# Optimization experiments

Hardware: AMD Instinct MI355X
Metric: run time of the kernel (lower is better)

## Reference

```python
import jax, jax.numpy as jnp
import numpy as np

L = 50
N_INIT = 3.5      # initial radius n
N_STEP = 0.5      # n_step
NUM_ADJ_PARM = 0.1
NUM_CANDS = 256   # candidate radii n + k*n_step


def _leaky(x):
    return jax.nn.leaky_relu(x, negative_slope=0.01)


def _conv(x, w, b):
    y = jax.lax.conv_general_dilated(x, w, (1, 1), 'VALID',
                                     dimension_numbers=('NCHW', 'OIHW', 'NCHW'))
    return y + b[None, :, None, None]


def _maxpool2(x):
    return jax.lax.reduce_window(x, -jnp.inf, jax.lax.max,
                                 (1, 1, 2, 2), (1, 1, 2, 2), 'VALID')


def _sage(x, adj, w_rel, b_rel, w_root):
    # PyG DenseSAGEConv: lin_rel(mean-agg) + lin_root(x), normalize=False
    agg = adj @ x
    deg = jnp.clip(jnp.sum(adj, axis=-1, keepdims=True), 1.0, None)
    return (agg / deg) @ w_rel.T + b_rel + x @ w_root.T


def _build_adj(h):
    # fused pairwise euclidean distance + radius threshold with retry:
    # smallest radius in {n + k*n_step} whose (directed) edge count >= 0.1*N
    g = h @ h.T                                   # [N,N] gram
    sq = jnp.diag(g)
    dist = jnp.sqrt(jnp.maximum(sq[:, None] - 2.0 * g + sq[None, :], 0.0))
    n = h.shape[0]
    eye = jnp.eye(n, dtype=bool)
    d_sorted = jnp.sort(jnp.where(eye, jnp.inf, dist).reshape(-1))
    cands = N_INIT + N_STEP * jnp.arange(NUM_CANDS, dtype=dist.dtype)
    counts = jnp.searchsorted(d_sorted, cands)    # edges with dist < cand
    thr = cands[jnp.argmax(counts >= NUM_ADJ_PARM * n)]
    A = ((dist < thr) & (~eye)).astype(h.dtype)
    return jax.lax.stop_gradient(A)               # edge list is non-diff in torch too


def _diff_pool(z, a, s):
    # PyG dense_diff_pool (link + entropy losses; only link loss l1 is returned)
    s = jax.nn.softmax(s, axis=-1)
    x = s.T @ z
    adj = s.T @ a @ s
    l1 = jnp.linalg.norm(a - s @ s.T) / (a.shape[0] * a.shape[1])
    return x, adj, l1


def setup_inputs() -> dict:
    key = jax.random.key(0)
    ks = jax.random.split(key, 19)
    def w(k, shape, scale=0.05):
        return scale * jax.random.normal(k, shape, dtype=jnp.float32)
    N = 4096  # bag size / number of graph nodes
    return {
        'x': jax.random.normal(ks[0], (1, N, 1, 28, 28), dtype=jnp.float32),
        'conv1_w': w(ks[1], (20, 1, 5, 5)),
        'conv1_b': w(ks[2], (20,)),
        'conv2_w': w(ks[3], (50, 20, 5, 5)),
        'conv2_b': w(ks[4], (50,)),
        'fc_w': w(ks[5], (50, 800)),
        'fc_b': w(ks[6], (50,)),
        'embd_rel_w': w(ks[7], (50, 50)),
        'embd_rel_b': w(ks[8], (50,)),
        'embd_root_w': w(ks[9], (50, 50)),
        'pool_rel_w': w(ks[10], (1, 50)),
        'pool_rel_b': w(ks[11], (1,)),
        'pool_root_w': w(ks[12], (1, 50)),
        'mlp_w': w(ks[13], (1, 1)),
        'mlp_b': w(ks[14], (1,)),
        'lin1_w': w(ks[15], (25, 50)),
        'lin1_b': w(ks[16], (25,)),
        'lin2_w': w(ks[17], (2, 25)),
        'lin2_b': w(ks[18], (2,)),
    }


def reference(x, conv1_w, conv1_b, conv2_w, conv2_b, fc_w, fc_b,
              embd_rel_w, embd_rel_b, embd_root_w,
              pool_rel_w, pool_rel_b, pool_root_w,
              mlp_w, mlp_b, lin1_w, lin1_b, lin2_w, lin2_b):
    xi = x[0]                                             # squeeze(0): [N,1,28,28]
    h = _maxpool2(jax.nn.relu(_conv(xi, conv1_w, conv1_b)))   # [N,20,12,12]
    h = _maxpool2(jax.nn.relu(_conv(h, conv2_w, conv2_b)))    # [N,50,4,4]
    h = h.reshape(h.shape[0], -1)                         # [N,800]
    h = jax.nn.relu(h @ fc_w.T + fc_b)                    # [N,50]
    A = _build_adj(h)                                     # [N,N] dense adjacency
    Z = _leaky(_sage(h, A, embd_rel_w, embd_rel_b, embd_root_w))   # [N,50]
    S = _leaky(_sage(h, A, pool_rel_w, pool_rel_b, pool_root_w))   # [N,1]
    S = _leaky(S @ mlp_w.T + mlp_b)                       # [N,1]
    Xp, adjp, l1 = _diff_pool(Z, A, S)                    # [1,50], [1,1]
    Xp = _leaky(_sage(Xp, adjp, embd_rel_w, embd_rel_b, embd_root_w))  # reuses gnn_embd
    v = Xp.reshape(-1)                                    # [50]
    v = _leaky(v @ lin1_w.T + lin1_b)                     # [25]
    v = _leaky(v @ lin2_w.T + lin2_b)                     # [2]
    p = jax.nn.softmax(v, axis=0)
    return jnp.max(p), jnp.argmax(p), l1
```

## Files before the change

### kernel.cpp

```cpp
#include <hip/hip_runtime.h>
#include <hip/hip_bf16.h>

#define AGG_OFF     0u
#define DEG_OFF     819200u
#define XP_OFF      835584u
#define HIST_OFF    835840u
#define SCAL_OFF    836992u
#define S_OFF       837120u
#define H_OFF       1048576u
#define HT_OFF      1867776u
#define SQ_OFF      2686976u

__global__ __launch_bounds__(256) void mil_init(unsigned int* __restrict__ w)
{
    w[(size_t)blockIdx.x * 256u + threadIdx.x] = 0u;
}

__global__ __launch_bounds__(256) void mil_cnn(
    const float* __restrict__ x, const float* __restrict__ w1, const float* __restrict__ b1,
    const float* __restrict__ w2, const float* __restrict__ b2,
    const float* __restrict__ fcw, const float* __restrict__ fcb,
    float* __restrict__ hout, float* __restrict__ hT, float* __restrict__ sqout)
{
    __shared__ __align__(16) float img[784];
    __shared__ float w1s[500];
    __shared__ float b1s[20];
    __shared__ float b2s[50];
    __shared__ __align__(16) float pool1[20*144];
    __shared__ float w2s[50*4*25];
    __shared__ __align__(16) float pool2[800];
    __shared__ float hloc[50];

    const int n = blockIdx.x;
    const int t = threadIdx.x;

    const float* xin = x + (size_t)n * 784;
    for (int i = t; i < 784; i += 256) img[i] = xin[i];
    for (int i = t; i < 500; i += 256) w1s[i] = w1[i];
    if (t < 20) b1s[t] = b1[t];
    { int u = t - 32; if (u >= 0 && u < 50) b2s[u] = b2[u]; }
    __syncthreads();

    if (t < 240) {
        const int c = t / 12, py = t % 12;
        float wr[25];
#pragma unroll
        for (int k = 0; k < 25; k++) wr[k] = w1s[c*25 + k];
        float acc0[24], acc1[24];
#pragma unroll
        for (int i = 0; i < 24; i++) { acc0[i] = 0.f; acc1[i] = 0.f; }
#pragma unroll
        for (int ky = 0; ky < 5; ky++) {
            const int yr = 2*py + ky;
            float ra[28], rb[28];
#pragma unroll
            for (int i = 0; i < 28; i++) ra[i] = img[yr*28 + i];
#pragma unroll
            for (int i = 0; i < 28; i++) rb[i] = img[yr*28 + 28 + i];
#pragma unroll
            for (int kx = 0; kx < 5; kx++) {
                const float wv = wr[ky*5 + kx];
#pragma unroll
                for (int xo = 0; xo < 24; xo++) {
                    acc0[xo] = fmaf(ra[xo+kx], wv, acc0[xo]);
                    acc1[xo] = fmaf(rb[xo+kx], wv, acc1[xo]);
                }
            }
        }
        const float bias = b1s[c];
#pragma unroll
        for (int px = 0; px < 12; px++) {
            float v = fmaxf(fmaxf(acc0[2*px], acc0[2*px+1]),
                            fmaxf(acc1[2*px], acc1[2*px+1]));
            pool1[c*144 + py*12 + px] = fmaxf(v + bias, 0.f);
        }
    }
    __syncthreads();

    float acc2[16];
#pragma unroll
    for (int i = 0; i < 16; i++) acc2[i] = 0.f;
    const int c2 = t / 4, py2 = t % 4;
    for (int cig = 0; cig < 5; cig++) {
        __syncthreads();
        for (int idx = t; idx < 5000; idx += 256) {
            const int cc = idx / 100, rem = idx % 100;
            w2s[idx] = w2[cc*500 + cig*100 + rem];
        }
        __syncthreads();
        if (t < 200) {
#pragma unroll
            for (int cl = 0; cl < 4; cl++) {
                const int cig4 = cig*4 + cl;
#pragma unroll
                for (int ky = 0; ky < 5; ky++) {
                    const int r = 2*py2 + ky;
                    float ra[12], rb[12];
#pragma unroll
                    for (int i = 0; i < 12; i++) ra[i] = pool1[cig4*144 + r*12 + i];
#pragma unroll
                    for (int i = 0; i < 12; i++) rb[i] = pool1[cig4*144 + (r+1)*12 + i];
#pragma unroll
                    for (int kx = 0; kx < 5; kx++) {
                        const float wv = w2s[(c2*4 + cl)*25 + ky*5 + kx];
#pragma unroll
                        for (int xo = 0; xo < 8; xo++) {
                            acc2[xo]   = fmaf(ra[xo+kx], wv, acc2[xo]);
                            acc2[8+xo] = fmaf(rb[xo+kx], wv, acc2[8+xo]);
                        }
                    }
                }
            }
        }
    }
    __syncthreads();
    if (t < 200) {
        const float bias = b2s[c2];
#pragma unroll
        for (int px = 0; px < 4; px++) {
            float v = fmaxf(fmaxf(acc2[2*px], acc2[2*px+1]),
                            fmaxf(acc2[8+2*px], acc2[8+2*px+1]));
            pool2[c2*16 + py2*4 + px] = fmaxf(v + bias, 0.f);
        }
    }
    __syncthreads();

    {
        const int wv = t >> 6, lane = t & 63;
        for (int o = wv; o < 50; o += 4) {
            float acc = 0.f;
#pragma unroll
            for (int r = 0; r < 13; r++) {
                const int k = r*64 + lane;
                if (k < 800) acc = fmaf(fcw[o*800 + k], pool2[k], acc);
            }
#pragma unroll
            for (int off = 32; off > 0; off >>= 1) acc += __shfl_xor(acc, off);
            if (lane == 0) hloc[o] = fmaxf(acc + fcb[o], 0.f);
        }
    }
    __syncthreads();
    if (t < 50) {
        const float v = hloc[t];
        hout[(size_t)n*50 + t] = v;
        hT[(size_t)t*4096 + n] = v;
    }
    if (t < 64) {
        float s = (t < 50) ? hloc[t]*hloc[t] : 0.f;
#pragma unroll
        for (int off = 32; off > 0; off >>= 1) s += __shfl_xor(s, off);
        if (t == 0) sqout[n] = s;
    }
}

__global__ __launch_bounds__(256) void mil_colsum(
    const float* __restrict__ hT, float* __restrict__ S)
{
    __shared__ float red[4];
    const int d = blockIdx.x, t = threadIdx.x;
    float s = 0.f;
    for (int nn = t; nn < 4096; nn += 256) s += hT[(size_t)d*4096 + nn];
#pragma unroll
    for (int off = 32; off > 0; off >>= 1) s += __shfl_xor(s, off);
    if ((t & 63) == 0) red[t >> 6] = s;
    __syncthreads();
    if (t == 0) S[d] = red[0] + red[1] + red[2] + red[3];
}

__global__ __launch_bounds__(256, 3) void mil_hist(
    const float* __restrict__ hT, const float* __restrict__ sq,
    unsigned int* __restrict__ hist)
{
    __shared__ __align__(16) float hiT[6400];
    __shared__ __align__(16) float hjT[6400];
    __shared__ float sqi[128], sqj[128];
    __shared__ unsigned int lh[257];

    const int t = threadIdx.x;
    const int i0 = blockIdx.x * 128, j0 = blockIdx.y * 128;

    for (int idx = t; idx < 6400; idx += 256) {
        const int c = idx >> 7, l = idx & 127;
        hiT[idx] = hT[(size_t)c*4096 + i0 + l];
        hjT[idx] = hT[(size_t)c*4096 + j0 + l];
    }
    if (t < 128) { sqi[t] = sq[i0 + t]; sqj[t] = sq[j0 + t]; }
    for (int idx = t; idx < 257; idx += 256) lh[idx] = 0;
    __syncthreads();

    const int ti = t >> 4, tj = t & 15;
    float acc[8][8];
#pragma unroll
    for (int a = 0; a < 8; a++)
#pragma unroll
        for (int b = 0; b < 8; b++) acc[a][b] = 0.f;

    for (int c = 0; c < 50; c++) {
        const float4 a0 = *(const float4*)&hiT[c*128 + ti*8];
        const float4 a1 = *(const float4*)&hiT[c*128 + ti*8 + 4];
        const float4 b0 = *(const float4*)&hjT[c*128 + tj*8];
        const float4 b1 = *(const float4*)&hjT[c*128 + tj*8 + 4];
        const float aa[8] = {a0.x,a0.y,a0.z,a0.w,a1.x,a1.y,a1.z,a1.w};
        const float bb[8] = {b0.x,b0.y,b0.z,b0.w,b1.x,b1.y,b1.z,b1.w};
#pragma unroll
        for (int a = 0; a < 8; a++)
#pragma unroll
            for (int b = 0; b < 8; b++)
                acc[a][b] = fmaf(aa[a], bb[b], acc[a][b]);
    }

    unsigned int cnt0 = 0;
#pragma unroll
    for (int a = 0; a < 8; a++) {
#pragma unroll
        for (int b = 0; b < 8; b++) {
            const int gi = i0 + ti*8 + a, gj = j0 + tj*8 + b;
            if (gi == gj) continue;
            const float d2 = sqi[ti*8+a] + sqj[tj*8+b] - 2.f*acc[a][b];
            const float d = sqrtf(fmaxf(d2, 0.f));
            int k = (int)floorf((d - 3.5f)*2.f) + 1;
            k = k < 0 ? 0 : (k > 256 ? 256 : k);
            if (k > 0   && d <  3.5f + 0.5f*(float)(k-1)) k--;
            if (k < 256 && d >= 3.5f + 0.5f*(float)k)     k++;
            if (k == 0) cnt0++;
            else atomicAdd(&lh[k], 1u);
        }
    }
#pragma unroll
    for (int off = 32; off > 0; off >>= 1) cnt0 += __shfl_xor(cnt0, off);
    if ((t & 63) == 0 && cnt0) atomicAdd(&lh[0], cnt0);
    __syncthreads();
    for (int idx = t; idx < 257; idx += 256)
        if (lh[idx]) atomicAdd(&hist[idx], lh[idx]);
}

__global__ void mil_scan(const unsigned int* __restrict__ hist, int* __restrict__ scal)
{
    if (threadIdx.x == 0) {
        unsigned long long cum = 0, nz = 0;
        int kc = -1;
        for (int k = 0; k < 256; k++) {
            cum += hist[k];
            if (kc < 0 && cum >= 410ull) { kc = k; nz = cum; }
        }
        if (kc < 0) { kc = 0; nz = hist[0]; }
        scal[0] = kc;
        scal[1] = (int)nz;
        scal[2] = (nz * 2ull > 16773120ull) ? 1 : 0;
    }
}

__global__ __launch_bounds__(256, 3) void mil_agg(
    const float* __restrict__ h, const float* __restrict__ hT, const float* __restrict__ sq,
    const int* __restrict__ scal, float* __restrict__ agg, float* __restrict__ deg)
{
    __shared__ __align__(16) float hiT[3200];
    __shared__ __align__(16) float hjT[3200];
    __shared__ float sqi[64], sqj[64];
    __shared__ __align__(16) float hsub[4096];
    __shared__ __align__(16) unsigned char mk[4096];

    const int t = threadIdx.x;
    const int i0 = blockIdx.x * 64;
    const float thr = 3.5f + 0.5f * (float)scal[0];
    const bool inv = (scal[2] != 0);

    for (int idx = t; idx < 3200; idx += 256) {
        const int c = idx >> 6, l = idx & 63;
        hiT[idx] = hT[(size_t)c*4096 + i0 + l];
    }
    if (t < 64) sqi[t] = sq[i0 + t];

    const int ti = t >> 4, tj = t & 15;
    const int il = t >> 2, dq = t & 3;
    float accum[16];
#pragma unroll
    for (int i = 0; i < 16; i++) accum[i] = 0.f;
    int degc = 0;

    for (int js = 0; js < 8; js++) {
        const int j0 = blockIdx.y * 512 + js * 64;
        __syncthreads();
        for (int idx = t; idx < 3200; idx += 256) {
            const int c = idx >> 6, l = idx & 63;
            hjT[idx] = hT[(size_t)c*4096 + j0 + l];
        }
        for (int idx = t; idx < 4096; idx += 256) {
            const int jj = idx >> 6, d = idx & 63;
            hsub[idx] = (d < 50) ? h[(size_t)(j0 + jj)*50 + d] : 0.f;
        }
        if (t < 64) sqj[t] = sq[j0 + t];
        __syncthreads();

        float acc[4][4];
#pragma unroll
        for (int a = 0; a < 4; a++)
#pragma unroll
            for (int b = 0; b < 4; b++) acc[a][b] = 0.f;
        for (int c = 0; c < 50; c++) {
            const float4 av = *(const float4*)&hiT[c*64 + ti*4];
            const float4 bv = *(const float4*)&hjT[c*64 + tj*4];
            const float aa[4] = {av.x, av.y, av.z, av.w};
            const float bb[4] = {bv.x, bv.y, bv.z, bv.w};
#pragma unroll
            for (int a = 0; a < 4; a++)
#pragma unroll
                for (int b = 0; b < 4; b++)
                    acc[a][b] = fmaf(aa[a], bb[b], acc[a][b]);
        }

#pragma unroll
        for (int b = 0; b < 4; b++) {
            unsigned char ob[4];
#pragma unroll
            for (int a = 0; a < 4; a++) {
                const int gi = i0 + ti*4 + a, gj = j0 + tj*4 + b;
                const float d2 = sqi[ti*4+a] + sqj[tj*4+b] - 2.f*acc[a][b];
                const float dd = sqrtf(fmaxf(d2, 0.f));
                const bool edge = (dd < thr);
                ob[a] = (gi != gj && (edge != inv)) ? 1 : 0;
            }
            *(uchar4*)&mk[(tj*4+b)*64 + ti*4] = make_uchar4(ob[0], ob[1], ob[2], ob[3]);
        }
        __syncthreads();

        for (int jj = 0; jj < 64; jj++) {
            const bool e = (mk[jj*64 + il] != 0);
            if (!__any(e)) continue;
            const float m = e ? 1.f : 0.f;
            if (e && dq == 0) degc++;
#pragma unroll
            for (int q = 0; q < 4; q++) {
                const float4 hv = *(const float4*)&hsub[jj*64 + dq*16 + q*4];
                accum[q*4+0] = fmaf(m, hv.x, accum[q*4+0]);
                accum[q*4+1] = fmaf(m, hv.y, accum[q*4+1]);
                accum[q*4+2] = fmaf(m, hv.z, accum[q*4+2]);
                accum[q*4+3] = fmaf(m, hv.w, accum[q*4+3]);
            }
        }
    }

    const int node = i0 + il;
#pragma unroll
    for (int q = 0; q < 4; q++)
#pragma unroll
        for (int rr = 0; rr < 4; rr++) {
            const int d = dq*16 + q*4 + rr;
            if (d < 50 && accum[q*4+rr] != 0.f)
                atomicAdd(&agg[(size_t)node*50 + d], accum[q*4+rr]);
        }
    if (dq == 0 && degc) atomicAdd(&deg[node], (float)degc);
}

__global__ __launch_bounds__(256) void mil_sage(
    const float* __restrict__ h, const float* __restrict__ agg, const float* __restrict__ deg,
    const float* __restrict__ S, const int* __restrict__ scal,
    const float* __restrict__ relw, const float* __restrict__ relb,
    const float* __restrict__ rootw, float* __restrict__ Xp)
{
    __shared__ float relT[2500];
    __shared__ float rootT[2500];
    __shared__ float rb[50];
    __shared__ float hn[250], mn[250], zb[250];
    const int t = threadIdx.x;
    const int nb = blockIdx.x * 5;
    const bool inv = (scal[2] != 0);

    for (int idx = t; idx < 2500; idx += 256) {
        const int d = idx / 50, c = idx % 50;
        relT[c*50 + d]  = relw[idx];
        rootT[c*50 + d] = rootw[idx];
    }
    if (t < 50) rb[t] = relb[t];
    if (t < 250) {
        const int nl = t / 50, d = t % 50;
        const int node = nb + nl;
        if (node < 4096) {
            const float hv = h[(size_t)node*50 + d];
            float av = agg[(size_t)node*50 + d];
            float dg = deg[node];
            if (inv) { av = S[d] - hv - av; dg = 4095.f - dg; }
            hn[t] = hv;
            mn[t] = av / fmaxf(dg, 1.f);
        } else { hn[t] = 0.f; mn[t] = 0.f; }
    }
    __syncthreads();
    if (t < 250) {
        const int nl = t / 50, d = t % 50;
        float z = rb[d];
        for (int c = 0; c < 50; c++) {
            z = fmaf(mn[nl*50 + c], relT[c*50 + d], z);
            z = fmaf(hn[nl*50 + c], rootT[c*50 + d], z);
        }
        z = z > 0.f ? z : 0.01f * z;
        zb[t] = (nb + nl < 4096) ? z : 0.f;
    }
    __syncthreads();
    if (t < 50) {
        float s = 0.f;
#pragma unroll
        for (int nl = 0; nl < 5; nl++) s += zb[nl*50 + t];
        atomicAdd(&Xp[t], s);
    }
}

__global__ void mil_final(
    const float* __restrict__ Xp, const int* __restrict__ scal,
    const float* __restrict__ relw, const float* __restrict__ relb,
    const float* __restrict__ rootw,
    const float* __restrict__ l1w, const float* __restrict__ l1b,
    const float* __restrict__ l2w, const float* __restrict__ l2b,
    float* __restrict__ out)
{
    __shared__ float xp[50], x2[50], v1[25], v2[2];
    const int t = threadIdx.x;
    if (t < 50) xp[t] = Xp[t];
    __syncthreads();
    const float adjp = (float)scal[1];
    const float dmax = fmaxf(adjp, 1.f);
    if (t < 50) {
        float z = relb[t];
        for (int c = 0; c < 50; c++) {
            const float mnc = (adjp * xp[c]) / dmax;
            z = fmaf(mnc,   relw[t*50 + c], z);
            z = fmaf(xp[c], rootw[t*50 + c], z);
        }
        x2[t] = z > 0.f ? z : 0.01f*z;
    }
    __syncthreads();
    if (t < 25) {
        float v = l1b[t];
        for (int c = 0; c < 50; c++) v = fmaf(l1w[t*50 + c], x2[c], v);
        v1[t] = v > 0.f ? v : 0.01f*v;
    }
    __syncthreads();
    if (t < 2) {
        float v = l2b[t];
        for (int c = 0; c < 25; c++) v = fmaf(l2w[t*25 + c], v1[c], v);
        v2[t] = v > 0.f ? v : 0.01f*v;
    }
    __syncthreads();
    if (t == 0) {
        const float a = v2[0], b = v2[1];
        const float mx = fmaxf(a, b);
        const float e0 = expf(a - mx), e1 = expf(b - mx);
        const float s = e0 + e1;
        const float p0 = e0 / s, p1 = e1 / s;
        const float pm = fmaxf(p0, p1);
        const float am = (p1 > p0) ? 1.f : 0.f;
        const int nnz = scal[1];
        const float l1v = sqrtf((float)(16777216 - nnz)) / 16777216.f;
        out[0] = pm;
        out[1] = am;
        out[2] = l1v;
    }
}

extern "C" void kernel_launch(void* const* d_in, const int* in_sizes, int n_in,
                              void* d_out, int out_size, void* d_ws, size_t ws_size,
                              hipStream_t stream)
{
    (void)in_sizes; (void)n_in; (void)out_size; (void)ws_size;
    const float* x     = (const float*)d_in[0];
    const float* w1    = (const float*)d_in[1];
    const float* b1    = (const float*)d_in[2];
    const float* w2    = (const float*)d_in[3];
    const float* b2    = (const float*)d_in[4];
    const float* fcw   = (const float*)d_in[5];
    const float* fcb   = (const float*)d_in[6];
    const float* relw  = (const float*)d_in[7];
    const float* relb  = (const float*)d_in[8];
    const float* rootw = (const float*)d_in[9];
    const float* l1w   = (const float*)d_in[15];
    const float* l1b   = (const float*)d_in[16];
    const float* l2w   = (const float*)d_in[17];
    const float* l2b   = (const float*)d_in[18];

    char* ws = (char*)d_ws;
    float* agg = (float*)(ws + AGG_OFF);
    float* deg = (float*)(ws + DEG_OFF);
    float* Xp  = (float*)(ws + XP_OFF);
    unsigned int* hist = (unsigned int*)(ws + HIST_OFF);
    int* scal  = (int*)(ws + SCAL_OFF);
    float* S   = (float*)(ws + S_OFF);
    float* h   = (float*)(ws + H_OFF);
    float* hT  = (float*)(ws + HT_OFF);
    float* sq  = (float*)(ws + SQ_OFF);

    mil_init<<<818, 256, 0, stream>>>((unsigned int*)d_ws);
    mil_cnn<<<4096, 256, 0, stream>>>(x, w1, b1, w2, b2, fcw, fcb, h, hT, sq);
    mil_colsum<<<50, 256, 0, stream>>>(hT, S);
    mil_hist<<<dim3(32, 32), 256, 0, stream>>>(hT, sq, hist);
    mil_scan<<<1, 64, 0, stream>>>(hist, scal);
    mil_agg<<<dim3(64, 8), 256, 0, stream>>>(h, hT, sq, scal, agg, deg);
    mil_sage<<<820, 256, 0, stream>>>(h, agg, deg, S, scal, relw, relb, rootw, Xp);
    mil_final<<<1, 64, 0, stream>>>(Xp, scal, relw, relb, rootw,
                                    l1w, l1b, l2w, l2b, (float*)d_out);
}
```

Baseline: 548.4 us.

## Run conv2 on MFMA with split-bf16 and aggregate histogram atomics per wavefront

Rewrites the second convolution as an implicit GEMM on bf16 MFMA instructions. Each fp32 operand is split into a high and a low bf16 part, and three MFMAs per tile approximate fp32 accuracy. A new prep kernel converts the conv2 weights into padded hi/lo bf16 arrays, which replaces the per-block shared-memory staging of weights. The histogram kernel now merges lanes that hit the same bin with ballot and popcount before each shared atomic, to cut atomic contention. The split-bf16 scheme drops the lo*lo term, so small numeric differences could shift radius-bin edges.

Measured after the change: 624.9 us. 14.0% more time.

```diff
diff --git a/kernel.cpp b/kernel.cpp
--- a/kernel.cpp
+++ b/kernel.cpp
@@ -10,15 +10,44 @@
 #define H_OFF       1048576u
 #define HT_OFF      1867776u
 #define SQ_OFF      2686976u
+#define W2H_OFF     2703360u
+#define W2L_OFF     2785280u
+
+typedef __attribute__((ext_vector_type(8))) short short8;
+typedef __attribute__((ext_vector_type(4))) float f32x4;
+
+__device__ __forceinline__ unsigned short f32_to_bf16_rne(float v) {
+    unsigned u = __float_as_uint(v);
+    unsigned r = u + 0x7FFFu + ((u >> 16) & 1u);
+    return (unsigned short)(r >> 16);
+}
+__device__ __forceinline__ float bf16_to_f32(unsigned short s) {
+    return __uint_as_float(((unsigned)s) << 16);
+}
 
 __global__ __launch_bounds__(256) void mil_init(unsigned int* __restrict__ w)
 {
     w[(size_t)blockIdx.x * 256u + threadIdx.x] = 0u;
 }
 
-__global__ __launch_bounds__(256) void mil_cnn(
+__global__ __launch_bounds__(256) void mil_wprep(
+    const float* __restrict__ w2, unsigned short* __restrict__ w2h,
+    unsigned short* __restrict__ w2l)
+{
+    const int gid = blockIdx.x * 256 + threadIdx.x;
+    const int k = gid % 640;
+    const int c = gid / 640;
+    const float v = (c < 50 && k < 500) ? w2[c*500 + k] : 0.f;
+    const unsigned short h = f32_to_bf16_rne(v);
+    const unsigned short l = f32_to_bf16_rne(v - bf16_to_f32(h));
+    w2h[gid] = h;
+    w2l[gid] = l;
+}
+
+__global__ __launch_bounds__(256, 3) void mil_cnn(
     const float* __restrict__ x, const float* __restrict__ w1, const float* __restrict__ b1,
-    const float* __restrict__ w2, const float* __restrict__ b2,
+    const unsigned short* __restrict__ w2h, const unsigned short* __restrict__ w2l,
+    const float* __restrict__ b2,
     const float* __restrict__ fcw, const float* __restrict__ fcb,
     float* __restrict__ hout, float* __restrict__ hT, float* __restrict__ sqout)
 {
@@ -27,9 +56,9 @@
     __shared__ float b1s[20];
     __shared__ float b2s[50];
     __shared__ __align__(16) float pool1[20*144];
-    __shared__ float w2s[50*4*25];
     __shared__ __align__(16) float pool2[800];
     __shared__ float hloc[50];
+    __shared__ int tabk[640];
 
     const int n = blockIdx.x;
     const int t = threadIdx.x;
@@ -39,6 +68,14 @@
     for (int i = t; i < 500; i += 256) w1s[i] = w1[i];
     if (t < 20) b1s[t] = b1[t];
     { int u = t - 32; if (u >= 0 && u < 50) b2s[u] = b2[u]; }
+    for (int kidx = t; kidx < 640; kidx += 256) {
+        int off = -1;
+        if (kidx < 500) {
+            const int ci = kidx / 25, r = kidx % 25;
+            off = ci*144 + (r/5)*12 + (r%5);
+        }
+        tabk[kidx] = off;
+    }
     __syncthreads();
 
     if (t < 240) {
@@ -77,50 +114,51 @@
     }
     __syncthreads();
 
-    float acc2[16];
-#pragma unroll
-    for (int i = 0; i < 16; i++) acc2[i] = 0.f;
-    const int c2 = t / 4, py2 = t % 4;
-    for (int cig = 0; cig < 5; cig++) {
-        __syncthreads();
-        for (int idx = t; idx < 5000; idx += 256) {
-            const int cc = idx / 100, rem = idx % 100;
-            w2s[idx] = w2[cc*500 + cig*100 + rem];
-        }
-        __syncthreads();
-        if (t < 200) {
-#pragma unroll
-            for (int cl = 0; cl < 4; cl++) {
-                const int cig4 = cig*4 + cl;
-#pragma unroll
-                for (int ky = 0; ky < 5; ky++) {
-                    const int r = 2*py2 + ky;
-                    float ra[12], rb[12];
-#pragma unroll
-                    for (int i = 0; i < 12; i++) ra[i] = pool1[cig4*144 + r*12 + i];
-#pragma unroll
-                    for (int i = 0; i < 12; i++) rb[i] = pool1[cig4*144 + (r+1)*12 + i];
-#pragma unroll
-                    for (int kx = 0; kx < 5; kx++) {
-                        const float wv = w2s[(c2*4 + cl)*25 + ky*5 + kx];
-#pragma unroll
-                        for (int xo = 0; xo < 8; xo++) {
-                            acc2[xo]   = fmaf(ra[xo+kx], wv, acc2[xo]);
-                            acc2[8+xo] = fmaf(rb[xo+kx], wv, acc2[8+xo]);
-                        }
-                    }
+    {
+        const int lane = t & 63, wv = t >> 6;
+        const int cL = lane & 15, g = lane >> 4;
+        const int srow = wv*16 + cL;
+        const int soff = (srow >> 3)*12 + (srow & 7);
+        f32x4 acc[4];
+#pragma unroll
+        for (int nn = 0; nn < 4; ++nn) acc[nn] = (f32x4){0.f, 0.f, 0.f, 0.f};
+
+        for (int kk = 0; kk < 20; ++kk) {
+            const int k0 = kk*32 + g*8;
+            short8 ah, al;
+#pragma unroll
+            for (int e = 0; e < 8; ++e) {
+                const int off = tabk[k0 + e];
+                const float v = (off >= 0) ? pool1[off + soff] : 0.f;
+                const unsigned short hh = f32_to_bf16_rne(v);
+                const unsigned short ll = f32_to_bf16_rne(v - bf16_to_f32(hh));
+                ah[e] = (short)hh;
+                al[e] = (short)ll;
+            }
+#pragma unroll
+            for (int nn = 0; nn < 4; ++nn) {
+                const int bo = (nn*16 + cL)*640 + k0;
+                const short8 bh = *(const short8*)(w2h + bo);
+                const short8 bl = *(const short8*)(w2l + bo);
+                acc[nn] = __builtin_amdgcn_mfma_f32_16x16x32_bf16(al, bh, acc[nn], 0, 0, 0);
+                acc[nn] = __builtin_amdgcn_mfma_f32_16x16x32_bf16(ah, bl, acc[nn], 0, 0, 0);
+                acc[nn] = __builtin_amdgcn_mfma_f32_16x16x32_bf16(ah, bh, acc[nn], 0, 0, 0);
+            }
+        }
+#pragma unroll
+        for (int nn = 0; nn < 4; ++nn) {
+            const float x0 = fmaxf(acc[nn].x, acc[nn].y);
+            const float x1 = fmaxf(acc[nn].z, acc[nn].w);
+            const float y0 = fmaxf(x0, __shfl_xor(x0, 32));
+            const float y1 = fmaxf(x1, __shfl_xor(x1, 32));
+            if (lane < 32) {
+                const int c = nn*16 + cL;
+                if (c < 50) {
+                    const float bias = b2s[c];
+                    pool2[c*16 + wv*4 + 2*g + 0] = fmaxf(y0 + bias, 0.f);
+                    pool2[c*16 + wv*4 + 2*g + 1] = fmaxf(y1 + bias, 0.f);
                 }
             }
-        }
-    }
-    __syncthreads();
-    if (t < 200) {
-        const float bias = b2s[c2];
-#pragma unroll
-        for (int px = 0; px < 4; px++) {
-            float v = fmaxf(fmaxf(acc2[2*px], acc2[2*px+1]),
-                            fmaxf(acc2[8+2*px], acc2[8+2*px+1]));
-            pool2[c2*16 + py2*4 + px] = fmaxf(v + bias, 0.f);
         }
     }
     __syncthreads();
@@ -177,6 +215,7 @@
     __shared__ unsigned int lh[257];
 
     const int t = threadIdx.x;
+    const int lane = t & 63;
     const int i0 = blockIdx.x * 128, j0 = blockIdx.y * 128;
 
     for (int idx = t; idx < 6400; idx += 256) {
@@ -209,26 +248,31 @@
                 acc[a][b] = fmaf(aa[a], bb[b], acc[a][b]);
     }
 
-    unsigned int cnt0 = 0;
 #pragma unroll
     for (int a = 0; a < 8; a++) {
 #pragma unroll
         for (int b = 0; b < 8; b++) {
             const int gi = i0 + ti*8 + a, gj = j0 + tj*8 + b;
-            if (gi == gj) continue;
-            const float d2 = sqi[ti*8+a] + sqj[tj*8+b] - 2.f*acc[a][b];
-            const float d = sqrtf(fmaxf(d2, 0.f));
-            int k = (int)floorf((d - 3.5f)*2.f) + 1;
-            k = k < 0 ? 0 : (k > 256 ? 256 : k);
-            if (k > 0   && d <  3.5f + 0.5f*(float)(k-1)) k--;
-            if (k < 256 && d >= 3.5f + 0.5f*(float)k)     k++;
-            if (k == 0) cnt0++;
-            else atomicAdd(&lh[k], 1u);
-        }
-    }
-#pragma unroll
-    for (int off = 32; off > 0; off >>= 1) cnt0 += __shfl_xor(cnt0, off);
-    if ((t & 63) == 0 && cnt0) atomicAdd(&lh[0], cnt0);
+            int kb = -1;
+            if (gi != gj) {
+                const float d2 = sqi[ti*8+a] + sqj[tj*8+b] - 2.f*acc[a][b];
+                const float d = sqrtf(fmaxf(d2, 0.f));
+                int k = (int)floorf((d - 3.5f)*2.f) + 1;
+                k = k < 0 ? 0 : (k > 256 ? 256 : k);
+                if (k > 0   && d <  3.5f + 0.5f*(float)(k-1)) k--;
+                if (k < 256 && d >= 3.5f + 0.5f*(float)k)     k++;
+                kb = k;
+            }
+            unsigned long long act = __ballot(kb >= 0);
+            while (act) {
+                const int src = __ffsll(act) - 1;
+                const int kk = __shfl(kb, src);
+                const unsigned long long same = __ballot(kb == kk) & act;
+                if (lane == src) atomicAdd(&lh[kk], (unsigned)__popcll(same));
+                act &= ~same;
+            }
+        }
+    }
     __syncthreads();
     for (int idx = t; idx < 257; idx += 256)
         if (lh[idx]) atomicAdd(&hist[idx], lh[idx]);
@@ -486,9 +530,12 @@
     float* h   = (float*)(ws + H_OFF);
     float* hT  = (float*)(ws + HT_OFF);
     float* sq  = (float*)(ws + SQ_OFF);
+    unsigned short* w2h = (unsigned short*)(ws + W2H_OFF);
+    unsigned short* w2l = (unsigned short*)(ws + W2L_OFF);
 
     mil_init<<<818, 256, 0, stream>>>((unsigned int*)d_ws);
-    mil_cnn<<<4096, 256, 0, stream>>>(x, w1, b1, w2, b2, fcw, fcb, h, hT, sq);
+    mil_wprep<<<160, 256, 0, stream>>>(w2, w2h, w2l);
+    mil_cnn<<<4096, 256, 0, stream>>>(x, w1, b1, w2h, w2l, b2, fcw, fcb, h, hT, sq);
     mil_colsum<<<50, 256, 0, stream>>>(hT, S);
     mil_hist<<<dim3(32, 32), 256, 0, stream>>>(hT, sq, hist);
     mil_scan<<<1, 64, 0, stream>>>(hist, scal);
```

## Cache per-pair radius bin bytes in hist pass to skip distance recompute in aggregation

Applied to the files above, without the earlier changes.

The histogram kernel now also writes a byte per (i,j) pair holding the clamped radius-bin index into a 16 MB workspace buffer. A new aggregation kernel reads these bytes and compares them against the chosen bin to build the adjacency mask, which avoids recomputing the Gram tile and distances a second time. The original recompute kernel stays as a fallback, used when the workspace is too small or the chosen bin saturates the byte range. The cost is 16 MB of extra global writes and reads plus an extra kernel launch that usually exits early.

New measurement: 542.4 us. Within noise of the previous version (-1.1%).

```diff
diff --git a/kernel.cpp b/kernel.cpp
--- a/kernel.cpp
+++ b/kernel.cpp
@@ -10,6 +10,8 @@
 #define H_OFF       1048576u
 #define HT_OFF      1867776u
 #define SQ_OFF      2686976u
+#define BYTES_OFF   2703360u
+#define WS_NEED     (2703360ull + 16777216ull)
 
 __global__ __launch_bounds__(256) void mil_init(unsigned int* __restrict__ w)
 {
@@ -169,7 +171,8 @@
 
 __global__ __launch_bounds__(256, 3) void mil_hist(
     const float* __restrict__ hT, const float* __restrict__ sq,
-    unsigned int* __restrict__ hist)
+    unsigned int* __restrict__ hist, unsigned char* __restrict__ bytesA,
+    const int wb)
 {
     __shared__ __align__(16) float hiT[6400];
     __shared__ __align__(16) float hjT[6400];
@@ -212,18 +215,28 @@
     unsigned int cnt0 = 0;
 #pragma unroll
     for (int a = 0; a < 8; a++) {
+        unsigned pk0 = 0, pk1 = 0;
 #pragma unroll
         for (int b = 0; b < 8; b++) {
             const int gi = i0 + ti*8 + a, gj = j0 + tj*8 + b;
-            if (gi == gj) continue;
-            const float d2 = sqi[ti*8+a] + sqj[tj*8+b] - 2.f*acc[a][b];
-            const float d = sqrtf(fmaxf(d2, 0.f));
-            int k = (int)floorf((d - 3.5f)*2.f) + 1;
-            k = k < 0 ? 0 : (k > 256 ? 256 : k);
-            if (k > 0   && d <  3.5f + 0.5f*(float)(k-1)) k--;
-            if (k < 256 && d >= 3.5f + 0.5f*(float)k)     k++;
-            if (k == 0) cnt0++;
-            else atomicAdd(&lh[k], 1u);
+            int kbyte = 255;
+            if (gi != gj) {
+                const float d2 = sqi[ti*8+a] + sqj[tj*8+b] - 2.f*acc[a][b];
+                const float d = sqrtf(fmaxf(d2, 0.f));
+                int k = (int)floorf((d - 3.5f)*2.f) + 1;
+                k = k < 0 ? 0 : (k > 256 ? 256 : k);
+                if (k > 0   && d <  3.5f + 0.5f*(float)(k-1)) k--;
+                if (k < 256 && d >= 3.5f + 0.5f*(float)k)     k++;
+                if (k == 0) cnt0++;
+                else atomicAdd(&lh[k], 1u);
+                kbyte = k < 255 ? k : 255;
+            }
+            if (b < 4) pk0 |= (unsigned)kbyte << (8*b);
+            else       pk1 |= (unsigned)kbyte << (8*(b-4));
+        }
+        if (wb) {
+            const int gi = i0 + ti*8 + a;
+            *(uint2*)&bytesA[(size_t)gi*4096 + j0 + tj*8] = make_uint2(pk0, pk1);
         }
     }
 #pragma unroll
@@ -247,12 +260,76 @@
         scal[0] = kc;
         scal[1] = (int)nz;
         scal[2] = (nz * 2ull > 16773120ull) ? 1 : 0;
-    }
-}
-
-__global__ __launch_bounds__(256, 3) void mil_agg(
+        scal[3] = (kc >= 255) ? 1 : 0;
+    }
+}
+
+__global__ __launch_bounds__(256) void mil_agg_b(
+    const float* __restrict__ h, const unsigned char* __restrict__ bytesA,
+    const int* __restrict__ scal, float* __restrict__ agg, float* __restrict__ deg)
+{
+    __shared__ __align__(16) unsigned char bL[64*528];
+    __shared__ __align__(16) float hsub[4096];
+    if (scal[3] != 0) return;
+    const int t = threadIdx.x;
+    const int i0 = blockIdx.x * 64;
+    const int jg = blockIdx.y * 512;
+    const int kc = scal[0];
+    const bool inv = (scal[2] != 0);
+
+    for (int idx = t; idx < 2048; idx += 256) {
+        const int r = idx >> 5, c = idx & 31;
+        *(uint4*)&bL[r*528 + c*16] =
+            *(const uint4*)&bytesA[(size_t)(i0 + r)*4096 + jg + c*16];
+    }
+
+    const int il = t >> 2, dq = t & 3;
+    const int gi = i0 + il;
+    float accum[16];
+#pragma unroll
+    for (int i = 0; i < 16; i++) accum[i] = 0.f;
+    int degc = 0;
+
+    for (int js = 0; js < 8; js++) {
+        __syncthreads();
+        for (int idx = t; idx < 4096; idx += 256) {
+            const int jj = idx >> 6, d = idx & 63;
+            hsub[idx] = (d < 50) ? h[(size_t)(jg + js*64 + jj)*50 + d] : 0.f;
+        }
+        __syncthreads();
+        const unsigned char* brow = &bL[il*528 + js*64];
+        const int jbase = jg + js*64;
+        for (int jj = 0; jj < 64; jj++) {
+            const bool e = (jbase + jj != gi) && ((brow[jj] <= kc) != inv);
+            if (!__any(e)) continue;
+            const float m = e ? 1.f : 0.f;
+            if (e && dq == 0) degc++;
+#pragma unroll
+            for (int q = 0; q < 4; q++) {
+                const float4 hv = *(const float4*)&hsub[jj*64 + dq*16 + q*4];
+                accum[q*4+0] = fmaf(m, hv.x, accum[q*4+0]);
+                accum[q*4+1] = fmaf(m, hv.y, accum[q*4+1]);
+                accum[q*4+2] = fmaf(m, hv.z, accum[q*4+2]);
+                accum[q*4+3] = fmaf(m, hv.w, accum[q*4+3]);
+            }
+        }
+    }
+
+#pragma unroll
+    for (int q = 0; q < 4; q++)
+#pragma unroll
+        for (int rr = 0; rr < 4; rr++) {
+            const int d = dq*16 + q*4 + rr;
+            if (d < 50 && accum[q*4+rr] != 0.f)
+                atomicAdd(&agg[(size_t)gi*50 + d], accum[q*4+rr]);
+        }
+    if (dq == 0 && degc) atomicAdd(&deg[gi], (float)degc);
+}
+
+__global__ __launch_bounds__(256, 3) void mil_agg_r(
     const float* __restrict__ h, const float* __restrict__ hT, const float* __restrict__ sq,
-    const int* __restrict__ scal, float* __restrict__ agg, float* __restrict__ deg)
+    const int* __restrict__ scal, float* __restrict__ agg, float* __restrict__ deg,
+    const int mode)
 {
     __shared__ __align__(16) float hiT[3200];
     __shared__ __align__(16) float hjT[3200];
@@ -260,6 +337,7 @@
     __shared__ __align__(16) float hsub[4096];
     __shared__ __align__(16) unsigned char mk[4096];
 
+    if (mode == 1 && scal[3] == 0) return;
     const int t = threadIdx.x;
     const int i0 = blockIdx.x * 64;
     const float thr = 3.5f + 0.5f * (float)scal[0];
@@ -460,7 +538,7 @@
                               void* d_out, int out_size, void* d_ws, size_t ws_size,
                               hipStream_t stream)
 {
-    (void)in_sizes; (void)n_in; (void)out_size; (void)ws_size;
+    (void)in_sizes; (void)n_in; (void)out_size;
     const float* x     = (const float*)d_in[0];
     const float* w1    = (const float*)d_in[1];
     const float* b1    = (const float*)d_in[2];
@@ -486,13 +564,21 @@
     float* h   = (float*)(ws + H_OFF);
     float* hT  = (float*)(ws + HT_OFF);
     float* sq  = (float*)(ws + SQ_OFF);
+    unsigned char* bytesA = (unsigned char*)(ws + BYTES_OFF);
+
+    const int have_bytes = (ws_size >= WS_NEED) ? 1 : 0;
 
     mil_init<<<818, 256, 0, stream>>>((unsigned int*)d_ws);
     mil_cnn<<<4096, 256, 0, stream>>>(x, w1, b1, w2, b2, fcw, fcb, h, hT, sq);
     mil_colsum<<<50, 256, 0, stream>>>(hT, S);
-    mil_hist<<<dim3(32, 32), 256, 0, stream>>>(hT, sq, hist);
+    mil_hist<<<dim3(32, 32), 256, 0, stream>>>(hT, sq, hist, bytesA, have_bytes);
     mil_scan<<<1, 64, 0, stream>>>(hist, scal);
-    mil_agg<<<dim3(64, 8), 256, 0, stream>>>(h, hT, sq, scal, agg, deg);
+    if (have_bytes) {
+        mil_agg_b<<<dim3(64, 8), 256, 0, stream>>>(h, bytesA, scal, agg, deg);
+        mil_agg_r<<<dim3(64, 8), 256, 0, stream>>>(h, hT, sq, scal, agg, deg, 1);
+    } else {
+        mil_agg_r<<<dim3(64, 8), 256, 0, stream>>>(h, hT, sq, scal, agg, deg, 0);
+    }
     mil_sage<<<820, 256, 0, stream>>>(h, agg, deg, S, scal, relw, relb, rootw, Xp);
     mil_final<<<1, 64, 0, stream>>>(Xp, scal, relw, relb, rootw,
                                     l1w, l1b, l2w, l2b, (float*)d_out);
```
